# Optimization experiments

Measured on AMD Instinct MI355X. Metric: run time of the kernel, lower is better.

The kernel has to match this reference:

```python
import jax, jax.numpy as jnp
import numpy as np

N_HEADS = 8
OUT_FEATURES = 64
LEAKY_SLOPE = 0.2
MASK_FILL = -1e9


def setup_inputs() -> dict:
    key = jax.random.key(0)
    k_h, k_adj, k_W, k_a = jax.random.split(key, 4)
    B, N, F_IN = 1, 4096, 128
    h = jax.random.normal(k_h, (B, N, F_IN), dtype=jnp.float32)
    adj_mat = jax.random.randint(k_adj, (N, N), 0, 2, dtype=jnp.int32)
    # glorot-style scaled params
    W = jax.random.normal(k_W, (F_IN, OUT_FEATURES * N_HEADS), dtype=jnp.float32) * (1.0 / np.sqrt(F_IN))
    a = jax.random.normal(k_a, (N_HEADS, 2 * OUT_FEATURES, 1), dtype=jnp.float32) * (1.0 / np.sqrt(2 * OUT_FEATURES))
    return {"h": h, "adj_mat": adj_mat, "W": W, "a": a}


def reference(h, adj_mat, W, a):
    B, N, _ = h.shape
    heads = a.shape[0]
    out = a.shape[1] // 2
    # linear transform + head split (same reshape order as tf.reshape)
    ht = jnp.reshape(h @ W, (-1, heads, N, out))            # (B, heads, N, out)
    # additive attention scores
    src = jnp.einsum('bhnf,hfo->bhno', ht, a[:, :out, :])    # (B, heads, N, 1)
    tgt = jnp.einsum('bhnf,hfo->bhno', ht, a[:, out:, :])    # (B, heads, N, 1)
    e = src + jnp.swapaxes(tgt, -1, -2)                      # (B, heads, N, N)
    e = jnp.where(e > 0, e, LEAKY_SLOPE * e)                 # leaky_relu
    e = jnp.where(adj_mat > 0, e, MASK_FILL)                 # adjacency mask
    attention = jax.nn.softmax(e, axis=-1)
    h_prime = attention @ ht                                 # (B, heads, N, out)
    return h_prime
```

## Files before the change

### kernel.cpp

```cpp
#include <hip/hip_runtime.h>
#include <stdint.h>

#define HT_STRIDE 262144
#define LOG2E 1.4426950408889634f

typedef __attribute__((ext_vector_type(8))) short bf16x8;
typedef __attribute__((ext_vector_type(4))) float f32x4;
typedef __attribute__((ext_vector_type(2))) float f32x2;

__device__ __forceinline__ unsigned short f2bf(float f) {
    unsigned int u = __float_as_uint(f);
    u += 0x7FFFu + ((u >> 16) & 1u);
    return (unsigned short)(u >> 16);
}

__device__ __forceinline__ float exp2_fast(float e) {
#if __has_builtin(__builtin_amdgcn_exp2f)
    return __builtin_amdgcn_exp2f(e);
#else
    return __expf(e * 0.6931471805599453f);
#endif
}

__global__ void __launch_bounds__(256) k_fused(const float* __restrict__ h,
                                               const int* __restrict__ adj,
                                               const float* __restrict__ W,
                                               const float* __restrict__ aW,
                                               float* __restrict__ ess,
                                               float* __restrict__ ets,
                                               unsigned short* __restrict__ htT2,
                                               unsigned int* __restrict__ abm) {
    __shared__ unsigned int ldsT[1024];
    __shared__ float hs[8][128];
    __shared__ float ldsA[64][66];
    __shared__ float redS[4][64];
    __shared__ float redT[4][64];
    const int t = threadIdx.x;

    if (blockIdx.x < 512) {
        const int lane = t & 63;
        const int w = t >> 6;
        const int sb = blockIdx.x >> 3;
        const int cq = blockIdx.x & 7;
        for (int rr = 0; rr < 16; ++rr) {
            const int* arow = adj + (sb * 64 + w * 16 + rr) * 4096 + cq * 512;
            int v[8];
            #pragma unroll
            for (int j = 0; j < 8; ++j) v[j] = arow[j * 64 + lane];
            #pragma unroll
            for (int j = 0; j < 8; ++j) {
                unsigned long long m = __ballot(v[j] > 0);
                if (lane < 2)
                    ldsT[(2 * j + lane) * 64 + rr * 4 + w] = (unsigned int)(m >> (lane * 32));
            }
        }
        __syncthreads();
        ((uint4*)(abm + (sb * 128 + cq * 16) * 64))[t] = ((uint4*)ldsT)[t];
    } else {
        const int bid2 = (int)blockIdx.x - 512;
        const int n0 = bid2 * 8;
        const int p0 = bid2 * 64;
        const int hd = p0 >> 12;
        const int m0 = p0 & 4095;

        {
            float4 v = ((const float4*)(h + n0 * 128))[t];
            int e = t * 4;
            int r = e >> 7, f = e & 127;
            hs[r][f + 0] = v.x; hs[r][f + 1] = v.y;
            hs[r][f + 2] = v.z; hs[r][f + 3] = v.w;
        }
        __syncthreads();

        float acc0[8], acc1[8];
        #pragma unroll
        for (int r = 0; r < 8; ++r) { acc0[r] = 0.f; acc1[r] = 0.f; }
        const float2* Wf = (const float2*)W;
        for (int f = 0; f < 128; ++f) {
            float2 wp = Wf[f * 256 + t];
            #pragma unroll
            for (int r = 0; r < 8; ++r) {
                float hv = hs[r][f];
                acc0[r] = fmaf(hv, wp.x, acc0[r]);
                acc1[r] = fmaf(hv, wp.y, acc1[r]);
            }
        }
        {
            const int ns = t >> 5;
            const int o = (2 * t) & 63;
            #pragma unroll
            for (int r = 0; r < 8; ++r) {
                *(float2*)&ldsA[r * 8 + ns][o] = make_float2(acc0[r], acc1[r]);
            }
        }
        __syncthreads();

        {
            const int r = t & 63, og = t >> 6;
            float sdot = 0.f, gdot = 0.f;
            #pragma unroll
            for (int k = 0; k < 16; ++k) {
                int o = og * 16 + k;
                float hv = ldsA[r][o];
                sdot = fmaf(hv, aW[hd * 128 + o], sdot);
                gdot = fmaf(hv, aW[hd * 128 + 64 + o], gdot);
            }
            redS[og][r] = sdot; redT[og][r] = gdot;
        }
        __syncthreads();
        if (t < 64) {
            float sp = (redS[0][t] + redS[1][t] + redS[2][t] + redS[3][t]) * LOG2E;
            ess[hd * 8192 + m0 + t]        = exp2_fast(sp);
            ess[hd * 8192 + 4096 + m0 + t] = exp2_fast(0.2f * sp);
        } else if (t < 128) {
            int r = t - 64;
            float tv = (redT[0][r] + redT[1][r] + redT[2][r] + redT[3][r]) * LOG2E;
            ets[hd * 8192 + m0 + r]        = exp2_fast(tv);
            ets[hd * 8192 + 4096 + m0 + r] = exp2_fast(0.2f * tv);
        }

        unsigned short* d = htT2 + (hd * 128 + (m0 >> 5)) * 2048;
        #pragma unroll
        for (int i = 0; i < 16; ++i) {
            int id = t + 256 * i;
            int mi = id & 31, o = (id >> 5) & 63, ct = id >> 11;
            d[ct * 2048 + o * 32 + mi] = f2bf(ldsA[mi + 32 * ct][o]);
        }
    }
}

__global__ void __launch_bounds__(256, 2) k_attn(const unsigned int* __restrict__ abm,
                                                 const unsigned short* __restrict__ htT2,
                                                 const float* __restrict__ ess,
                                                 const float* __restrict__ ets,
                                                 float* __restrict__ out) {
    __shared__ __align__(16) float smem[13056];

    const int t = threadIdx.x;
    const int kq = t >> 6;
    const int lane = t & 63;
    const int li = lane & 15;
    const int quad = lane >> 4;
    const int head = blockIdx.x & 7;
    const int s64 = blockIdx.x >> 3;
    const int i0 = s64 * 64;

    {
        const float4* esrc = (const float4*)(ets + head * 8192);
        float4* edst = (float4*)smem;
        #pragma unroll
        for (int i = 0; i < 8; ++i) edst[t + 256 * i] = esrc[t + 256 * i];
    }

    f32x2 esv[4], es2v[4];
    #pragma unroll
    for (int g2 = 0; g2 < 4; ++g2) {
        float e1 = ess[head * 8192 + i0 + 16 * g2 + li];
        float e2 = ess[head * 8192 + 4096 + i0 + 16 * g2 + li];
        esv[g2]  = (f32x2){e1, e1};
        es2v[g2] = (f32x2){e2, e2};
    }

    f32x4 acc[16];
    #pragma unroll
    for (int i = 0; i < 16; ++i) acc[i] = (f32x4){0.f, 0.f, 0.f, 0.f};
    f32x4 apd[4];
    #pragma unroll
    for (int g2 = 0; g2 < 4; ++g2) apd[g2] = (f32x4){0.f, 0.f, 0.f, 0.f};

    const uint4 onesw = {0x3F803F80u, 0x3F803F80u, 0x3F803F80u, 0x3F803F80u};
    const bf16x8 aones = __builtin_bit_cast(bf16x8, onesw);
    const unsigned int lohalf = 0x0000FFFFu;

    const uint4* ap  = (const uint4*)(htT2 + head * HT_STRIDE) + (li * 4 + quad);
    const uint4* bmp = (const uint4*)(abm + s64 * 8192 + li * 4);

    __syncthreads();

    const int c0 = kq * 32;
    #pragma unroll 2
    for (int ci = 0; ci < 32; ++ci) {
        const int c = c0 + ci;
        uint4 av0 = ap[c * 256 + 0];
        uint4 av1 = ap[c * 256 + 64];
        uint4 av2 = ap[c * 256 + 128];
        uint4 av3 = ap[c * 256 + 192];
        uint4 bw = bmp[c * 16];

        const float4* etp  = (const float4*)(smem + c * 32 + quad * 8);
        const float4* et2p = (const float4*)(smem + 4096 + c * 32 + quad * 8);
        float4 ta = etp[0],  tb = etp[1];
        float4 ua = et2p[0], ub = et2p[1];
        const f32x2 etq[4]  = {(f32x2){ta.x, ta.y}, (f32x2){ta.z, ta.w},
                               (f32x2){tb.x, tb.y}, (f32x2){tb.z, tb.w}};
        const f32x2 et2q[4] = {(f32x2){ua.x, ua.y}, (f32x2){ua.z, ua.w},
                               (f32x2){ub.x, ub.y}, (f32x2){ub.z, ub.w}};

        const unsigned int wb[4] = {bw.x, bw.y, bw.z, bw.w};
        #pragma unroll
        for (int g2 = 0; g2 < 4; ++g2) {
            const unsigned int wq = wb[g2] >> (quad * 8);
            unsigned int pk[4];
            #pragma unroll
            for (int m = 0; m < 4; ++m) {
                f32x2 p1 = etq[m] * esv[g2];
                f32x2 p2 = et2q[m] * es2v[g2];
                float w0 = fmaxf(p1[0], p2[0]);
                float w1 = fmaxf(p1[1], p2[1]);
                unsigned int pkm;
                asm("v_cvt_pk_bf16_f32 %0, %1, %2" : "=v"(pkm) : "v"(w0), "v"(w1));
                unsigned int lo, hi, msk;
                asm("v_bfe_i32 %0, %1, %2, 1" : "=v"(lo) : "v"(wq), "n"(2 * m));
                asm("v_bfe_i32 %0, %1, %2, 1" : "=v"(hi) : "v"(wq), "n"(2 * m + 1));
                asm("v_bfi_b32 %0, %1, %2, %3" : "=v"(msk) : "v"(lohalf), "v"(lo), "v"(hi));
                pk[m] = pkm & msk;
            }
            uint4 bv; bv.x = pk[0]; bv.y = pk[1]; bv.z = pk[2]; bv.w = pk[3];
            bf16x8 bfrag = __builtin_bit_cast(bf16x8, bv);
            apd[g2] = __builtin_amdgcn_mfma_f32_16x16x32_bf16(aones, bfrag, apd[g2], 0, 0, 0);
            acc[g2 * 4 + 0] = __builtin_amdgcn_mfma_f32_16x16x32_bf16(__builtin_bit_cast(bf16x8, av0), bfrag, acc[g2 * 4 + 0], 0, 0, 0);
            acc[g2 * 4 + 1] = __builtin_amdgcn_mfma_f32_16x16x32_bf16(__builtin_bit_cast(bf16x8, av1), bfrag, acc[g2 * 4 + 1], 0, 0, 0);
            acc[g2 * 4 + 2] = __builtin_amdgcn_mfma_f32_16x16x32_bf16(__builtin_bit_cast(bf16x8, av2), bfrag, acc[g2 * 4 + 2], 0, 0, 0);
            acc[g2 * 4 + 3] = __builtin_amdgcn_mfma_f32_16x16x32_bf16(__builtin_bit_cast(bf16x8, av3), bfrag, acc[g2 * 4 + 3], 0, 0, 0);
        }
    }

    __syncthreads();
    if (kq != 0) {
        float* cb = smem + ((kq - 1) * 64 + lane) * 68;
        #pragma unroll
        for (int i = 0; i < 16; ++i) ((f32x4*)cb)[i] = acc[i];
        #pragma unroll
        for (int g2 = 0; g2 < 4; ++g2) cb[64 + g2] = apd[g2][0];
    }
    __syncthreads();
    if (kq == 0) {
        float pd[4] = {apd[0][0], apd[1][0], apd[2][0], apd[3][0]};
        #pragma unroll
        for (int q = 0; q < 3; ++q) {
            const float* cb = smem + (q * 64 + lane) * 68;
            #pragma unroll
            for (int i = 0; i < 16; ++i) acc[i] += ((const f32x4*)cb)[i];
            #pragma unroll
            for (int g2 = 0; g2 < 4; ++g2) pd[g2] += cb[64 + g2];
        }
        #pragma unroll
        for (int g2 = 0; g2 < 4; ++g2) {
            const float rd = 1.0f / pd[g2];
            float4* op = (float4*)(out + head * HT_STRIDE + (i0 + 16 * g2 + li) * 64);
            #pragma unroll
            for (int f = 0; f < 4; ++f) {
                f32x4 a = acc[g2 * 4 + f];
                op[f * 4 + quad] = make_float4(a[0] * rd, a[1] * rd, a[2] * rd, a[3] * rd);
            }
        }
    }
}

extern "C" void kernel_launch(void* const* d_in, const int* in_sizes, int n_in,
                              void* d_out, int out_size, void* d_ws, size_t ws_size,
                              hipStream_t stream) {
    const float* h   = (const float*)d_in[0];
    const int*   adj = (const int*)d_in[1];
    const float* W   = (const float*)d_in[2];
    const float* aW  = (const float*)d_in[3];
    float* out = (float*)d_out;

    char* ws = (char*)d_ws;
    float* ess = (float*)(ws);
    float* ets = (float*)(ws + 262144);
    unsigned int*   abm  = (unsigned int*)(ws + 524288);
    unsigned short* htT2 = (unsigned short*)(ws + 2621440);

    hipLaunchKernelGGL(k_fused, dim3(1024), dim3(256), 0, stream,
                       h, adj, W, aW, ess, ets, htT2, abm);
    hipLaunchKernelGGL(k_attn,  dim3(512),  dim3(256), 0, stream,
                       abm, htT2, ess, ets, out);
}
```

Baseline: 150.9 us.

## Interleave fused kernel block roles, prefetch W, widen attention blocks to 8 waves

The first kernel now interleaves adjacency-packing blocks and projection blocks by block parity, so both kinds of work are spread across the GPU at once. The projection loop prefetches W in groups of four rows to hide load latency. The attention kernel doubles its block size to 512 threads, so each wave covers 16 column chunks instead of 32, and merges the per-wave partial results with a tree reduction through LDS. This buys more parallelism per block at the cost of more LDS, more barriers, and tighter register limits from launch bounds (512,4).

```diff
diff --git a/kernel.cpp b/kernel.cpp
--- a/kernel.cpp
+++ b/kernel.cpp
@@ -37,11 +37,12 @@
     __shared__ float redT[4][64];
     const int t = threadIdx.x;
 
-    if (blockIdx.x < 512) {
+    if ((blockIdx.x & 1) == 0) {
+        const int eid = (int)blockIdx.x >> 1;
         const int lane = t & 63;
         const int w = t >> 6;
-        const int sb = blockIdx.x >> 3;
-        const int cq = blockIdx.x & 7;
+        const int sb = eid >> 3;
+        const int cq = eid & 7;
         for (int rr = 0; rr < 16; ++rr) {
             const int* arow = adj + (sb * 64 + w * 16 + rr) * 4096 + cq * 512;
             int v[8];
@@ -57,7 +58,7 @@
         __syncthreads();
         ((uint4*)(abm + (sb * 128 + cq * 16) * 64))[t] = ((uint4*)ldsT)[t];
     } else {
-        const int bid2 = (int)blockIdx.x - 512;
+        const int bid2 = (int)blockIdx.x >> 1;
         const int n0 = bid2 * 8;
         const int p0 = bid2 * 64;
         const int hd = p0 >> 12;
@@ -76,14 +77,26 @@
         #pragma unroll
         for (int r = 0; r < 8; ++r) { acc0[r] = 0.f; acc1[r] = 0.f; }
         const float2* Wf = (const float2*)W;
-        for (int f = 0; f < 128; ++f) {
-            float2 wp = Wf[f * 256 + t];
-            #pragma unroll
-            for (int r = 0; r < 8; ++r) {
-                float hv = hs[r][f];
-                acc0[r] = fmaf(hv, wp.x, acc0[r]);
-                acc1[r] = fmaf(hv, wp.y, acc1[r]);
-            }
+        float2 wpb[4];
+        #pragma unroll
+        for (int j = 0; j < 4; ++j) wpb[j] = Wf[j * 256 + t];
+        for (int fb = 0; fb < 32; ++fb) {
+            const int fn = ((fb + 1) & 31) * 4;
+            float2 wn[4];
+            #pragma unroll
+            for (int j = 0; j < 4; ++j) wn[j] = Wf[(fn + j) * 256 + t];
+            #pragma unroll
+            for (int j = 0; j < 4; ++j) {
+                const int f = fb * 4 + j;
+                #pragma unroll
+                for (int r = 0; r < 8; ++r) {
+                    float hv = hs[r][f];
+                    acc0[r] = fmaf(hv, wpb[j].x, acc0[r]);
+                    acc1[r] = fmaf(hv, wpb[j].y, acc1[r]);
+                }
+            }
+            #pragma unroll
+            for (int j = 0; j < 4; ++j) wpb[j] = wn[j];
         }
         {
             const int ns = t >> 5;
@@ -129,12 +142,12 @@
     }
 }
 
-__global__ void __launch_bounds__(256, 2) k_attn(const unsigned int* __restrict__ abm,
+__global__ void __launch_bounds__(512, 4) k_attn(const unsigned int* __restrict__ abm,
                                                  const unsigned short* __restrict__ htT2,
                                                  const float* __restrict__ ess,
                                                  const float* __restrict__ ets,
                                                  float* __restrict__ out) {
-    __shared__ __align__(16) float smem[13056];
+    __shared__ __align__(16) float smem[17408];
 
     const int t = threadIdx.x;
     const int kq = t >> 6;
@@ -149,7 +162,7 @@
         const float4* esrc = (const float4*)(ets + head * 8192);
         float4* edst = (float4*)smem;
         #pragma unroll
-        for (int i = 0; i < 8; ++i) edst[t + 256 * i] = esrc[t + 256 * i];
+        for (int i = 0; i < 4; ++i) edst[t + 512 * i] = esrc[t + 512 * i];
     }
 
     f32x2 esv[4], es2v[4];
@@ -177,9 +190,9 @@
 
     __syncthreads();
 
-    const int c0 = kq * 32;
-    #pragma unroll 2
-    for (int ci = 0; ci < 32; ++ci) {
+    const int c0 = kq * 16;
+    #pragma unroll 1
+    for (int ci = 0; ci < 16; ++ci) {
         const int c = c0 + ci;
         uint4 av0 = ap[c * 256 + 0];
         uint4 av1 = ap[c * 256 + 64];
@@ -225,28 +238,58 @@
         }
     }
 
-    __syncthreads();
-    if (kq != 0) {
-        float* cb = smem + ((kq - 1) * 64 + lane) * 68;
+    float pdv[4] = {apd[0][0], apd[1][0], apd[2][0], apd[3][0]};
+    __syncthreads();
+
+    if (kq >= 4) {
+        float* cb = smem + ((kq - 4) * 64 + lane) * 68;
         #pragma unroll
         for (int i = 0; i < 16; ++i) ((f32x4*)cb)[i] = acc[i];
         #pragma unroll
-        for (int g2 = 0; g2 < 4; ++g2) cb[64 + g2] = apd[g2][0];
+        for (int g2 = 0; g2 < 4; ++g2) cb[64 + g2] = pdv[g2];
+    }
+    __syncthreads();
+    if (kq < 4) {
+        const float* cb = smem + (kq * 64 + lane) * 68;
+        #pragma unroll
+        for (int i = 0; i < 16; ++i) acc[i] += ((const f32x4*)cb)[i];
+        #pragma unroll
+        for (int g2 = 0; g2 < 4; ++g2) pdv[g2] += cb[64 + g2];
+    }
+    __syncthreads();
+    if (kq == 2 || kq == 3) {
+        float* cb = smem + ((kq - 2) * 64 + lane) * 68;
+        #pragma unroll
+        for (int i = 0; i < 16; ++i) ((f32x4*)cb)[i] = acc[i];
+        #pragma unroll
+        for (int g2 = 0; g2 < 4; ++g2) cb[64 + g2] = pdv[g2];
+    }
+    __syncthreads();
+    if (kq < 2) {
+        const float* cb = smem + (kq * 64 + lane) * 68;
+        #pragma unroll
+        for (int i = 0; i < 16; ++i) acc[i] += ((const f32x4*)cb)[i];
+        #pragma unroll
+        for (int g2 = 0; g2 < 4; ++g2) pdv[g2] += cb[64 + g2];
+    }
+    __syncthreads();
+    if (kq == 1) {
+        float* cb = smem + lane * 68;
+        #pragma unroll
+        for (int i = 0; i < 16; ++i) ((f32x4*)cb)[i] = acc[i];
+        #pragma unroll
+        for (int g2 = 0; g2 < 4; ++g2) cb[64 + g2] = pdv[g2];
     }
     __syncthreads();
     if (kq == 0) {
-        float pd[4] = {apd[0][0], apd[1][0], apd[2][0], apd[3][0]};
-        #pragma unroll
-        for (int q = 0; q < 3; ++q) {
-            const float* cb = smem + (q * 64 + lane) * 68;
-            #pragma unroll
-            for (int i = 0; i < 16; ++i) acc[i] += ((const f32x4*)cb)[i];
-            #pragma unroll
-            for (int g2 = 0; g2 < 4; ++g2) pd[g2] += cb[64 + g2];
-        }
+        const float* cb = smem + lane * 68;
+        #pragma unroll
+        for (int i = 0; i < 16; ++i) acc[i] += ((const f32x4*)cb)[i];
+        #pragma unroll
+        for (int g2 = 0; g2 < 4; ++g2) pdv[g2] += cb[64 + g2];
         #pragma unroll
         for (int g2 = 0; g2 < 4; ++g2) {
-            const float rd = 1.0f / pd[g2];
+            const float rd = 1.0f / pdv[g2];
             float4* op = (float4*)(out + head * HT_STRIDE + (i0 + 16 * g2 + li) * 64);
             #pragma unroll
             for (int f = 0; f < 4; ++f) {
@@ -274,6 +317,6 @@
 
     hipLaunchKernelGGL(k_fused, dim3(1024), dim3(256), 0, stream,
                        h, adj, W, aW, ess, ets, htT2, abm);
-    hipLaunchKernelGGL(k_attn,  dim3(512),  dim3(256), 0, stream,
+    hipLaunchKernelGGL(k_attn,  dim3(512),  dim3(512), 0, stream,
                        abm, htT2, ess, ets, out);
 }
```

New measurement: 211.6 us. 40.2% more time.
